# Performance work log

Measured on AMD Instinct MI355X. Metric: run time of the kernel, lower is better.

The kernel has to match this reference:

```python
import jax, jax.numpy as jnp
import numpy as np

IMG_LEN, TXT_LEN = 50, 76
SEQ = IMG_LEN + TXT_LEN
D_IMG, D, VOCAB = 768, 512, 49408
N_LAYERS = 2
EPS = 1e-5


def _layer_norm(x, g, b):
    m = jnp.mean(x, axis=-1, keepdims=True)
    v = jnp.mean(jnp.square(x - m), axis=-1, keepdims=True)
    return (x - m) * jax.lax.rsqrt(v + EPS) * g + b


def setup_inputs() -> dict:
    key = jax.random.key(0)
    ks = jax.random.split(key, 20)
    s = 0.02
    inp = {
        "image_embeddings": jax.random.normal(ks[0], (32, IMG_LEN, D_IMG), jnp.float32),
        "caption_ids": jax.random.randint(ks[1], (32, TXT_LEN), 0, VOCAB),
        "token_emb": jax.random.normal(ks[2], (VOCAB, D), jnp.float32) * s,
        "pos_emb": jax.random.normal(ks[3], (TXT_LEN, D), jnp.float32) * s,
        "ff0_w": jax.random.normal(ks[4], (D_IMG, D), jnp.float32) * s,
        "ff0_b": jnp.zeros((D,), jnp.float32),
        "wq": jax.random.normal(ks[5], (D, D), jnp.float32) * s,
        "wq_b": jnp.zeros((D,), jnp.float32),
        "wk": jax.random.normal(ks[6], (D, D), jnp.float32) * s,
        "wk_b": jnp.zeros((D,), jnp.float32),
        "wv": jax.random.normal(ks[7], (D, D), jnp.float32) * s,
        "wv_b": jnp.zeros((D,), jnp.float32),
        "ln_g": jnp.ones((D,), jnp.float32),
        "ln_b": jnp.zeros((D,), jnp.float32),
        "ff1_w": jax.random.normal(ks[8], (D, D), jnp.float32) * s,
        "ff1_b": jnp.zeros((D,), jnp.float32),
        "ff2_w": jax.random.normal(ks[9], (D, VOCAB), jnp.float32) * s,
        "ff2_b": jnp.zeros((VOCAB,), jnp.float32),
    }
    return inp


def reference(image_embeddings, caption_ids, token_emb, pos_emb, ff0_w, ff0_b,
              wq, wq_b, wk, wk_b, wv, wv_b, ln_g, ln_b, ff1_w, ff1_b, ff2_w, ff2_b):
    # prefix-causal mask: fully visible image prefix, causal over the rest
    mask = jnp.tril(jnp.ones((SEQ, SEQ), jnp.float32)).at[:, :IMG_LEN].set(1.0)

    img = image_embeddings @ ff0_w + ff0_b                      # [B,50,512]
    txt = token_emb[caption_ids] + pos_emb[None, :, :]          # [B,76,512]
    x = jnp.concatenate([img, txt], axis=1)                     # [B,126,512]
    x = _layer_norm(x, ln_g, ln_b)

    for _ in range(N_LAYERS):  # shared params across layers (as in source)
        res1 = x
        q = x @ wq + wq_b
        k = x @ wk + wk_b
        v = x @ wv + wv_b
        sims = jnp.einsum('bqd,bkd->bqk', q, k) / np.sqrt(D).astype(np.float32)
        sims = jnp.where(mask == 0, -1e9, sims)
        attn = jax.nn.softmax(sims, axis=-1)
        x = jnp.einsum('bqk,bkd->bqd', attn, v)
        x = _layer_norm(x + res1, ln_g, ln_b)
        res2 = x
        x = x @ ff1_w + ff1_b
        x = _layer_norm(x + res2, ln_g, ln_b)

    logits = x @ ff2_w + ff2_b                                  # [B,126,VOCAB]
    return logits[:, IMG_LEN:, :]                               # [B,76,VOCAB]
```

## Files before the change

### kernel.cpp

```cpp
#include <hip/hip_runtime.h>

typedef unsigned short ushort_t;
typedef __attribute__((ext_vector_type(8))) short short8;
typedef __attribute__((ext_vector_type(4))) float f32x4;
typedef __attribute__((ext_vector_type(4))) unsigned short bf4;
typedef __attribute__((ext_vector_type(8))) unsigned short bf8v;

__device__ __forceinline__ ushort_t f2bf(float f) {
    union { float f; unsigned u; } v; v.f = f;
    unsigned r = v.u + 0x7FFFu + ((v.u >> 16) & 1u);
    return (ushort_t)(r >> 16);
}

__device__ __forceinline__ void g2lds16(const ushort_t* g, ushort_t* l) {
    __builtin_amdgcn_global_load_lds(
        (const __attribute__((address_space(1))) void*)g,
        (__attribute__((address_space(3))) void*)l, 16, 0, 0);
}

#define LDT 72

__global__ __launch_bounds__(512) void gemm_big(
    const ushort_t* __restrict__ xb, const ushort_t* __restrict__ B,
    float* __restrict__ C, const float* __restrict__ bias,
    int K, int ldb, int ldc, int validM)
{
    __shared__ __attribute__((aligned(16))) ushort_t As[2][256 * 64];
    __shared__ __attribute__((aligned(16))) ushort_t Bs[2][256 * 64];

    const int tid = threadIdx.x;
    const int lane = tid & 63;
    const int wave = tid >> 6;
    const int wr = wave >> 2;
    const int wc = wave & 3;
    int tN, tM;
    {
        const int lin = blockIdx.x + blockIdx.y * gridDim.x;
        const int TM = gridDim.y;
        const int full = gridDim.x >> 3;
        const int per = TM << 3;
        const int g = lin / per;
        if (g < full) {
            const int rem = lin - g * per;
            tM = rem >> 3;
            tN = (g << 3) + (rem & 7);
        } else {
            const int rem = lin - full * per;
            const int w = gridDim.x - (full << 3);
            tM = rem / w;
            tN = (full << 3) + rem - tM * w;
        }
    }
    const int n0 = tN * 256;
    const ushort_t* Bbase = B + (long)n0 * ldb;

    f32x4 acc[8][4];
#pragma unroll
    for (int m = 0; m < 8; m++)
#pragma unroll
        for (int n = 0; n < 4; n++) acc[m][n] = (f32x4)0.f;

    auto STAGE = [&](int buf, int ks) {
#pragma unroll
        for (int i = 0; i < 4; i++) {
            int ch = i * 512 + tid;
            int row = ch >> 3, c16 = ch & 7;
            int c16s = c16 ^ (row & 7);
            int gr = tM * 256 + row;
            if (gr > 2431) gr = 2431;
            int bb = gr / 76;
            int xrow = bb * 126 + 50 + (gr - bb * 76);
            g2lds16(xb + (long)xrow * 512 + ks + (c16s << 3),
                    &As[buf][(i * 512 + wave * 64) * 8]);
        }
#pragma unroll
        for (int i = 0; i < 4; i++) {
            int ch = i * 512 + tid;
            int row = ch >> 3, c16 = ch & 7;
            int c16s = c16 ^ (row & 7);
            g2lds16(Bbase + (long)row * ldb + ks + (c16s << 3),
                    &Bs[buf][(i * 512 + wave * 64) * 8]);
        }
    };

    const int nt = K >> 6;
    STAGE(0, 0);
    for (int t = 0; t < nt; ++t) {
        if (t + 1 < nt) {
            STAGE((t + 1) & 1, (t + 1) << 6);
            asm volatile("s_waitcnt vmcnt(8)" ::: "memory");
        } else {
            asm volatile("s_waitcnt vmcnt(0)" ::: "memory");
        }
        asm volatile("s_barrier" ::: "memory");

        const ushort_t* Ac = As[t & 1];
        const ushort_t* Bc = Bs[t & 1];
        __builtin_amdgcn_s_setprio(1);
#pragma unroll
        for (int ksub = 0; ksub < 2; ksub++) {
            const int kk = ksub * 32 + ((lane >> 4) << 3);
            const int kc = kk >> 3;
            short8 af[8], bfr[4];
#pragma unroll
            for (int m = 0; m < 8; m++) {
                const int r = (wr << 7) + m * 16 + (lane & 15);
                af[m] = *(const short8*)(Ac + r * 64 + ((kc ^ (r & 7)) << 3));
            }
#pragma unroll
            for (int n = 0; n < 4; n++) {
                const int r = (wc << 6) + n * 16 + (lane & 15);
                bfr[n] = *(const short8*)(Bc + r * 64 + ((kc ^ (r & 7)) << 3));
            }
#pragma unroll
            for (int m = 0; m < 8; m++)
#pragma unroll
                for (int n = 0; n < 4; n++)
                    acc[m][n] = __builtin_amdgcn_mfma_f32_16x16x32_bf16(
                        af[m], bfr[n], acc[m][n], 0, 0, 0);
        }
        __builtin_amdgcn_s_setprio(0);
        asm volatile("s_barrier" ::: "memory");
    }

    const int rb = (wr << 7) + ((lane >> 4) << 2);
    const int cb = (wc << 6) + (lane & 15);
#pragma unroll
    for (int m = 0; m < 8; m++) {
#pragma unroll
        for (int i = 0; i < 4; i++) {
            int r = tM * 256 + rb + m * 16 + i;
            if (r >= validM) continue;
#pragma unroll
            for (int n = 0; n < 4; n++) {
                int cg = n0 + cb + n * 16;
                C[(long)r * ldc + cg] = acc[m][n][i] + bias[cg];
            }
        }
    }
}

__global__ __launch_bounds__(512) void ff1_fused(
    ushort_t* __restrict__ xbg, const ushort_t* __restrict__ ff1T,
    const float* __restrict__ bias, float* __restrict__ xg,
    const float* __restrict__ ln_g, const float* __restrict__ ln_b)
{
    __shared__ __attribute__((aligned(16))) ushort_t As[32 * 64];
    __shared__ __attribute__((aligned(16))) ushort_t Bs[512 * 64];
    __shared__ float redm[4 * 32];
    __shared__ float reds[4 * 32];

    const int tid = threadIdx.x;
    const int lane = tid & 63;
    const int wave = tid >> 6;
    const int wr = wave >> 2;
    const int wc = wave & 3;
    const int r0 = blockIdx.x << 5;

    f32x4 acc[8];
#pragma unroll
    for (int n = 0; n < 8; n++) acc[n] = (f32x4)0.f;

    auto STAGE = [&](int ks) {
#pragma unroll
        for (int i = 0; i < 9; i++) {
            int cb = i * 512 + wave * 64;
            if (cb >= 4352) continue;
            int ch = cb + lane;
            if (cb < 256) {
                int row = ch >> 3, c16 = ch & 7;
                int c16s = c16 ^ (row & 7);
                g2lds16(xbg + (long)(r0 + row) * 512 + ks + (c16s << 3),
                        &As[cb * 8]);
            } else {
                int bch = ch - 256;
                int row = bch >> 3, c16 = bch & 7;
                int c16s = c16 ^ (row & 7);
                g2lds16(ff1T + (long)row * 512 + ks + (c16s << 3),
                        &Bs[(cb - 256) * 8]);
            }
        }
    };

    for (int ks = 0; ks < 512; ks += 64) {
        if (ks) asm volatile("s_barrier" ::: "memory");
        STAGE(ks);
        asm volatile("s_waitcnt vmcnt(0)" ::: "memory");
        asm volatile("s_barrier" ::: "memory");

        __builtin_amdgcn_s_setprio(1);
#pragma unroll
        for (int ksub = 0; ksub < 2; ksub++) {
            const int kc = ksub * 4 + (lane >> 4);
            short8 af;
            {
                const int r = (wr << 4) + (lane & 15);
                af = *(const short8*)(As + r * 64 + ((kc ^ (r & 7)) << 3));
            }
            short8 bfr[8];
#pragma unroll
            for (int n = 0; n < 8; n++) {
                const int r = (wc << 7) + n * 16 + (lane & 15);
                bfr[n] = *(const short8*)(Bs + r * 64 + ((kc ^ (r & 7)) << 3));
            }
#pragma unroll
            for (int n = 0; n < 8; n++)
                acc[n] = __builtin_amdgcn_mfma_f32_16x16x32_bf16(
                    af, bfr[n], acc[n], 0, 0, 0);
        }
        __builtin_amdgcn_s_setprio(0);
    }

    float gg[8], bb2[8], bi[8];
#pragma unroll
    for (int n = 0; n < 8; n++) {
        int d = (wc << 7) + n * 16 + (lane & 15);
        gg[n] = ln_g[d];
        bb2[n] = ln_b[d];
        bi[n] = bias[d];
    }
    float vv[4][8];
#pragma unroll
    for (int i = 0; i < 4; i++) {
        const int rl = (wr << 4) + ((lane >> 4) << 2) + i;
        const long xrow = (long)(r0 + rl) << 9;
        float s = 0.f, sq = 0.f;
#pragma unroll
        for (int n = 0; n < 8; n++) {
            int d = (wc << 7) + n * 16 + (lane & 15);
            float v = acc[n][i] + bi[n] + xg[xrow + d];
            vv[i][n] = v;
            s += v; sq += v * v;
        }
#pragma unroll
        for (int o = 8; o >= 1; o >>= 1) { s += __shfl_xor(s, o); sq += __shfl_xor(sq, o); }
        if ((lane & 15) == 0) {
            redm[wc * 32 + rl] = s;
            reds[wc * 32 + rl] = sq;
        }
    }
    __syncthreads();
#pragma unroll
    for (int i = 0; i < 4; i++) {
        const int rl = (wr << 4) + ((lane >> 4) << 2) + i;
        float S = redm[rl] + redm[32 + rl] + redm[64 + rl] + redm[96 + rl];
        float SQ = reds[rl] + reds[32 + rl] + reds[64 + rl] + reds[96 + rl];
        float mean = S * (1.f / 512.f);
        float var = SQ * (1.f / 512.f) - mean * mean;
        float inv = rsqrtf(var + 1e-5f);
        const long xrow = (long)(r0 + rl) << 9;
#pragma unroll
        for (int n = 0; n < 8; n++) {
            int d = (wc << 7) + n * 16 + (lane & 15);
            float y = (vv[i][n] - mean) * inv * gg[n] + bb2[n];
            xg[xrow + d] = y;
            xbg[xrow + d] = f2bf(y);
        }
    }
}

__global__ __launch_bounds__(512) void attn_fused(
    const ushort_t* __restrict__ qkv, float* __restrict__ xg,
    ushort_t* __restrict__ xbg, const float* __restrict__ ln_g,
    const float* __restrict__ ln_b)
{
    __shared__ __attribute__((aligned(16))) ushort_t smem[41984];
    ushort_t* Vs = smem;
    ushort_t* Ps = smem + 32768;
    float* redm = (float*)(smem + 40960);
    float* reds = redm + 256;
    ushort_t* Qs = smem;
    ushort_t* Ks = smem + 8192;

    const int tid = threadIdx.x;
    const int lane = tid & 63;
    const int wave = tid >> 6;
    const int wr = wave >> 2;
    const int wc = wave & 3;
    const int qh = blockIdx.x;
    const int b  = blockIdx.y;
    const long qbase = ((long)(b * 126) + qh * 64) * 1536;
    const long kbase = (long)(b * 126) * 1536 + 512;
    const long vbase = (long)(b * 126) * 1536 + 1024;
    const float rsqd = 0.044194173824159216f;

    f32x4 acc[2][2];
#pragma unroll
    for (int m = 0; m < 2; m++)
#pragma unroll
        for (int n = 0; n < 2; n++) acc[m][n] = (f32x4)0.f;

    auto SQK = [&](int buf, int ks) {
        {
            int ch = tid;
            int row = ch >> 3, c16 = ch & 7;
            int c16s = c16 ^ (row & 7);
            g2lds16(qkv + qbase + (long)row * 1536 + ks + (c16s << 3),
                    Qs + buf * 4096 + (wave * 64) * 8);
        }
#pragma unroll
        for (int i = 0; i < 2; i++) {
            int ch = i * 512 + tid;
            int row = ch >> 3, c16 = ch & 7;
            int c16s = c16 ^ (row & 7);
            g2lds16(qkv + kbase + (long)row * 1536 + ks + (c16s << 3),
                    Ks + buf * 8192 + (i * 512 + wave * 64) * 8);
        }
    };

    SQK(0, 0);
    for (int t = 0; t < 8; ++t) {
        if (t < 7) {
            SQK((t + 1) & 1, (t + 1) << 6);
            asm volatile("s_waitcnt vmcnt(3)" ::: "memory");
        } else {
            asm volatile("s_waitcnt vmcnt(0)" ::: "memory");
        }
        asm volatile("s_barrier" ::: "memory");
        const ushort_t* Qc = Qs + (t & 1) * 4096;
        const ushort_t* Kc = Ks + (t & 1) * 8192;
#pragma unroll
        for (int ksub = 0; ksub < 2; ksub++) {
            const int kc = ksub * 4 + (lane >> 4);
            short8 af[2], bfr[2];
#pragma unroll
            for (int m = 0; m < 2; m++) {
                const int r = (wr << 5) + m * 16 + (lane & 15);
                af[m] = *(const short8*)(Qc + r * 64 + ((kc ^ (r & 7)) << 3));
            }
#pragma unroll
            for (int n = 0; n < 2; n++) {
                const int r = (wc << 5) + n * 16 + (lane & 15);
                bfr[n] = *(const short8*)(Kc + r * 64 + ((kc ^ (r & 7)) << 3));
            }
#pragma unroll
            for (int m = 0; m < 2; m++)
#pragma unroll
                for (int n = 0; n < 2; n++)
                    acc[m][n] = __builtin_amdgcn_mfma_f32_16x16x32_bf16(
                        af[m], bfr[n], acc[m][n], 0, 0, 0);
        }
        asm volatile("s_barrier" ::: "memory");
    }

    float rm[2][4];
#pragma unroll
    for (int m = 0; m < 2; m++) {
#pragma unroll
        for (int i = 0; i < 4; i++) {
            const int rl = (wr << 5) + m * 16 + ((lane >> 4) << 2) + i;
            const int q = qh * 64 + rl;
            float mx = -3.0e38f;
#pragma unroll
            for (int n = 0; n < 2; n++) {
                int j = (wc << 5) + n * 16 + (lane & 15);
                bool ok = (j < 126) && ((j < 50) || (j <= q));
                float s = acc[m][n][i] * rsqd;
                acc[m][n][i] = ok ? s : -3.0e38f;
                if (ok) mx = fmaxf(mx, s);
            }
#pragma unroll
            for (int o = 8; o >= 1; o >>= 1) mx = fmaxf(mx, __shfl_xor(mx, o));
            rm[m][i] = mx;
        }
    }
    if ((lane & 15) == 0) {
#pragma unroll
        for (int m = 0; m < 2; m++)
#pragma unroll
            for (int i = 0; i < 4; i++) {
                int rl = (wr << 5) + m * 16 + ((lane >> 4) << 2) + i;
                redm[wc * 64 + rl] = rm[m][i];
            }
    }
    __syncthreads();
    float rs[2][4];
#pragma unroll
    for (int m = 0; m < 2; m++) {
#pragma unroll
        for (int i = 0; i < 4; i++) {
            const int rl = (wr << 5) + m * 16 + ((lane >> 4) << 2) + i;
            float M = fmaxf(fmaxf(redm[rl], redm[64 + rl]),
                            fmaxf(redm[128 + rl], redm[192 + rl]));
            float sum = 0.f;
#pragma unroll
            for (int n = 0; n < 2; n++) {
                float s = acc[m][n][i];
                float e = (s > -1.0e37f) ? expf(s - M) : 0.f;
                acc[m][n][i] = e;
                sum += e;
            }
#pragma unroll
            for (int o = 8; o >= 1; o >>= 1) sum += __shfl_xor(sum, o);
            rs[m][i] = sum;
        }
    }
    if ((lane & 15) == 0) {
#pragma unroll
        for (int m = 0; m < 2; m++)
#pragma unroll
            for (int i = 0; i < 4; i++) {
                int rl = (wr << 5) + m * 16 + ((lane >> 4) << 2) + i;
                reds[wc * 64 + rl] = rs[m][i];
            }
    }
    __syncthreads();
#pragma unroll
    for (int m = 0; m < 2; m++) {
#pragma unroll
        for (int i = 0; i < 4; i++) {
            const int rl = (wr << 5) + m * 16 + ((lane >> 4) << 2) + i;
            float S = reds[rl] + reds[64 + rl] + reds[128 + rl] + reds[192 + rl];
            float inv = 1.f / S;
#pragma unroll
            for (int n = 0; n < 2; n++) {
                int j = (wc << 5) + n * 16 + (lane & 15);
                int c = j >> 3;
                Ps[rl * 128 + ((c ^ (rl & 7)) << 3) + (j & 7)] =
                    f2bf(acc[m][n][i] * inv);
            }
        }
    }
    __syncthreads();

    f32x4 po[2][8];
#pragma unroll
    for (int m = 0; m < 2; m++)
#pragma unroll
        for (int n = 0; n < 8; n++) po[m][n] = (f32x4)0.f;

    for (int jc = 0; jc < 2; jc++) {
#pragma unroll
        for (int q8 = 0; q8 < 16; q8++) {
            int qid = q8 * 512 + tid;
            int d = qid & 511, jq = qid >> 9;
            const ushort_t* vp = qkv + vbase + (long)(jc * 64 + jq * 4) * 1536 + d;
            bf4 p;
            p[0] = vp[0];
            p[1] = vp[1536];
            p[2] = vp[3072];
            p[3] = vp[4608];
            *(bf4*)(Vs + d * 64 + (((jq >> 1) ^ (d & 7)) << 3) + ((jq & 1) << 2)) = p;
        }
        __syncthreads();
#pragma unroll
        for (int ksub = 0; ksub < 2; ksub++) {
            const int kc = ksub * 4 + (lane >> 4);
            short8 af[2], bv[8];
#pragma unroll
            for (int m = 0; m < 2; m++) {
                const int r = (wr << 5) + m * 16 + (lane & 15);
                const int c = jc * 8 + kc;
                af[m] = *(const short8*)(Ps + r * 128 + ((c ^ (r & 7)) << 3));
            }
#pragma unroll
            for (int n = 0; n < 8; n++) {
                const int r = (wc << 7) + n * 16 + (lane & 15);
                bv[n] = *(const short8*)(Vs + r * 64 + ((kc ^ (r & 7)) << 3));
            }
#pragma unroll
            for (int m = 0; m < 2; m++)
#pragma unroll
                for (int n = 0; n < 8; n++)
                    po[m][n] = __builtin_amdgcn_mfma_f32_16x16x32_bf16(
                        af[m], bv[n], po[m][n], 0, 0, 0);
        }
        __syncthreads();
    }

    float gg[8], bb2[8];
#pragma unroll
    for (int n = 0; n < 8; n++) {
        int d = (wc << 7) + n * 16 + (lane & 15);
        gg[n] = ln_g[d];
        bb2[n] = ln_b[d];
    }
#pragma unroll
    for (int m = 0; m < 2; m++) {
#pragma unroll
        for (int i = 0; i < 4; i++) {
            const int rl = (wr << 5) + m * 16 + ((lane >> 4) << 2) + i;
            const int q = qh * 64 + rl;
            const long xrow = ((long)(b * 126 + q)) << 9;
            float s = 0.f, sq = 0.f;
#pragma unroll
            for (int n = 0; n < 8; n++) {
                int d = (wc << 7) + n * 16 + (lane & 15);
                float v = po[m][n][i] + xg[xrow + d];
                po[m][n][i] = v;
                s += v; sq += v * v;
            }
#pragma unroll
            for (int o = 8; o >= 1; o >>= 1) { s += __shfl_xor(s, o); sq += __shfl_xor(sq, o); }
            if ((lane & 15) == 0) {
                redm[wc * 64 + rl] = s;
                reds[wc * 64 + rl] = sq;
            }
        }
    }
    __syncthreads();
#pragma unroll
    for (int m = 0; m < 2; m++) {
#pragma unroll
        for (int i = 0; i < 4; i++) {
            const int rl = (wr << 5) + m * 16 + ((lane >> 4) << 2) + i;
            const int q = qh * 64 + rl;
            if (q >= 126) continue;
            float S = redm[rl] + redm[64 + rl] + redm[128 + rl] + redm[192 + rl];
            float SQ = reds[rl] + reds[64 + rl] + reds[128 + rl] + reds[192 + rl];
            float mean = S * (1.f / 512.f);
            float var = SQ * (1.f / 512.f) - mean * mean;
            float inv = rsqrtf(var + 1e-5f);
            const long xrow = ((long)(b * 126 + q)) << 9;
#pragma unroll
            for (int n = 0; n < 8; n++) {
                int d = (wc << 7) + n * 16 + (lane & 15);
                float y = (po[m][n][i] - mean) * inv * gg[n] + bb2[n];
                xg[xrow + d] = y;
                xbg[xrow + d] = f2bf(y);
            }
        }
    }
}

template <int BSRC, int SWZ, int NT>
__global__ __launch_bounds__(256) void gemm_bf16(
    const ushort_t* __restrict__ A, const void* __restrict__ Bv,
    float* __restrict__ C, ushort_t* __restrict__ Cb,
    const float* __restrict__ bias,
    int K, int lda, int ldb, int ldc,
    long sA, long sB, long sC,
    int validM, float scale)
{
    constexpr int LS = (BSRC == 0) ? 64 : LDT;
    constexpr int NBUF = (BSRC == 0) ? 2 : 1;
    __shared__ __attribute__((aligned(16))) ushort_t As[NBUF * 128 * LS];
    __shared__ __attribute__((aligned(16))) ushort_t Bs[NBUF * 128 * LS];

    const int tid = threadIdx.x;
    const int lane = tid & 63;
    const int wave = tid >> 6;
    const int wr = wave >> 1, wc = wave & 1;
    int tN = blockIdx.x, tM = blockIdx.y;
    const int bz = blockIdx.z;
    if (SWZ) {
        const int lin = blockIdx.x + blockIdx.y * gridDim.x;
        const int TM = gridDim.y;
        const int full = gridDim.x >> 3;
        const int per = TM << 3;
        const int g = lin / per;
        if (g < full) {
            const int rem = lin - g * per;
            tM = rem >> 3;
            tN = (g << 3) + (rem & 7);
        } else {
            const int rem = lin - full * per;
            const int w = gridDim.x - (full << 3);
            tM = rem / w;
            tN = (full << 3) + rem - tM * w;
        }
    }
    const int n0 = tN * 128;

    const ushort_t* Abase = A + (long)bz * sA + (long)tM * 128 * lda;
    const ushort_t* Bb = (BSRC == 0)
        ? (const ushort_t*)Bv + (long)bz * sB + (long)n0 * ldb : nullptr;
    const float* Bf = (BSRC == 1)
        ? (const float*)Bv + (long)bz * sB : nullptr;

    f32x4 acc[4][4];
#pragma unroll
    for (int m = 0; m < 4; m++)
#pragma unroll
        for (int n = 0; n < 4; n++) acc[m][n] = (f32x4)0.f;

    if (BSRC == 0) {
        auto STAGE = [&](int buf, int ks) {
            ushort_t* Ad = As + buf * (128 * 64);
            ushort_t* Bd = Bs + buf * (128 * 64);
#pragma unroll
            for (int i = 0; i < 4; i++) {
                int ch = wave * 256 + i * 64 + lane;
                int row = ch >> 3, c16 = ch & 7;
                int c16s = c16 ^ (row & 7);
                g2lds16(Abase + (long)row * lda + ks + (c16s << 3),
                        Ad + (wave * 256 + i * 64) * 8);
            }
#pragma unroll
            for (int i = 0; i < 4; i++) {
                int ch = wave * 256 + i * 64 + lane;
                int row = ch >> 3, c16 = ch & 7;
                int c16s = c16 ^ (row & 7);
                g2lds16(Bb + (long)row * ldb + ks + (c16s << 3),
                        Bd + (wave * 256 + i * 64) * 8);
            }
        };

        const int nt = K >> 6;
        STAGE(0, 0);
        for (int t = 0; t < nt; ++t) {
            if (t + 1 < nt) {
                STAGE((t + 1) & 1, (t + 1) << 6);
                asm volatile("s_waitcnt vmcnt(8)" ::: "memory");
            } else {
                asm volatile("s_waitcnt vmcnt(0)" ::: "memory");
            }
            asm volatile("s_barrier" ::: "memory");

            const ushort_t* Ac = As + (t & 1) * (128 * 64);
            const ushort_t* Bc = Bs + (t & 1) * (128 * 64);
#pragma unroll
            for (int ksub = 0; ksub < 2; ksub++) {
                const int kk = ksub * 32 + ((lane >> 4) << 3);
                const int kc = kk >> 3;
                short8 af[4], bfr[4];
#pragma unroll
                for (int m = 0; m < 4; m++) {
                    const int r = (wr << 6) + m * 16 + (lane & 15);
                    af[m] = *(const short8*)(Ac + r * 64 + ((kc ^ (r & 7)) << 3));
                }
#pragma unroll
                for (int n = 0; n < 4; n++) {
                    const int r = (wc << 6) + n * 16 + (lane & 15);
                    bfr[n] = *(const short8*)(Bc + r * 64 + ((kc ^ (r & 7)) << 3));
                }
#pragma unroll
                for (int m = 0; m < 4; m++)
#pragma unroll
                    for (int n = 0; n < 4; n++)
                        acc[m][n] = __builtin_amdgcn_mfma_f32_16x16x32_bf16(
                            af[m], bfr[n], acc[m][n], 0, 0, 0);
            }
            asm volatile("s_barrier" ::: "memory");
        }
    } else {
        for (int ks = 0; ks < K; ks += 64) {
            short8 ar[4];
#pragma unroll
            for (int i = 0; i < 4; i++) {
                int ch = wave * 256 + i * 64 + lane;
                int row = ch >> 3, c16 = ch & 7;
                ar[i] = *(const short8*)(Abase + (long)row * lda + ks + (c16 << 3));
            }
            bf4 pk[8];
#pragma unroll
            for (int q = 0; q < 8; q++) {
                int qid = q * 256 + tid;
                int n = qid & 127, kq = qid >> 7;
                const float* wp = Bf + (long)(ks + kq * 4) * ldb + n0 + n;
                bf4 p;
                p[0] = f2bf(wp[0]);
                p[1] = f2bf(wp[ldb]);
                p[2] = f2bf(wp[2 * (long)ldb]);
                p[3] = f2bf(wp[3 * (long)ldb]);
                pk[q] = p;
            }
            if (ks) __syncthreads();
#pragma unroll
            for (int i = 0; i < 4; i++) {
                int ch = wave * 256 + i * 64 + lane;
                int row = ch >> 3, c16 = ch & 7;
                *(short8*)(As + row * LS + (c16 << 3)) = ar[i];
            }
#pragma unroll
            for (int q = 0; q < 8; q++) {
                int qid = q * 256 + tid;
                int n = qid & 127, kq = qid >> 7;
                *(bf4*)(Bs + n * LS + (kq << 2)) = pk[q];
            }
            __syncthreads();

#pragma unroll
            for (int ksub = 0; ksub < 2; ksub++) {
                const int kk = ksub * 32 + ((lane >> 4) << 3);
                short8 af[4], bfr[4];
#pragma unroll
                for (int m = 0; m < 4; m++) {
                    const int r = (wr << 6) + m * 16 + (lane & 15);
                    af[m] = *(const short8*)(As + r * LS + kk);
                }
#pragma unroll
                for (int n = 0; n < 4; n++) {
                    const int r = (wc << 6) + n * 16 + (lane & 15);
                    bfr[n] = *(const short8*)(Bs + r * LS + kk);
                }
#pragma unroll
                for (int m = 0; m < 4; m++)
#pragma unroll
                    for (int n = 0; n < 4; n++)
                        acc[m][n] = __builtin_amdgcn_mfma_f32_16x16x32_bf16(
                            af[m], bfr[n], acc[m][n], 0, 0, 0);
            }
            if (ks + 64 < K) __syncthreads();
        }
    }

    const int rb = (wr << 6) + ((lane >> 4) << 2);
    const int cb = (wc << 6) + (lane & 15);
#pragma unroll
    for (int m = 0; m < 4; m++) {
#pragma unroll
        for (int i = 0; i < 4; i++) {
            int r = tM * 128 + rb + m * 16 + i;
            if (r >= validM) continue;
#pragma unroll
            for (int n = 0; n < 4; n++) {
                int cg = n0 + cb + n * 16;
                float v = acc[m][n][i] * scale + (bias ? bias[cg] : 0.f);
                long off = (long)bz * sC + (long)r * ldc + cg;
                if (C) {
                    if (NT) __builtin_nontemporal_store(v, &C[off]);
                    else    C[off] = v;
                }
                if (Cb) Cb[off] = f2bf(v);
            }
        }
    }
}

__global__ __launch_bounds__(256) void transpose_bf(
    const float* __restrict__ in, ushort_t* __restrict__ out, int R, int C)
{
    __shared__ float t[32][33];
    int c0 = blockIdx.x << 5, r0 = blockIdx.y << 5;
    int tx = threadIdx.x, ty = threadIdx.y;
#pragma unroll
    for (int i = 0; i < 4; i++)
        t[ty + i * 8][tx] = in[(long)(r0 + ty + i * 8) * C + c0 + tx];
    __syncthreads();
#pragma unroll
    for (int i = 0; i < 4; i++)
        out[(long)(c0 + ty + i * 8) * R + r0 + tx] = f2bf(t[tx][ty + i * 8]);
}

__global__ __launch_bounds__(256) void transpose_ff2(
    const float* __restrict__ in, ushort_t* __restrict__ out)
{
    __shared__ float t[64][65];
    const int c0 = blockIdx.x << 6;
    const int r0 = blockIdx.y << 6;
    const int tx = threadIdx.x & 63, ty = threadIdx.x >> 6;
#pragma unroll
    for (int i = 0; i < 16; i++) {
        int r = ty + i * 4;
        t[r][tx] = in[(long)(r0 + r) * 49408 + c0 + tx];
    }
    __syncthreads();
#pragma unroll
    for (int i = 0; i < 16; i++) {
        int r = ty + i * 4;
        out[(long)(c0 + r) * 512 + r0 + tx] = f2bf(t[tx][r]);
    }
}

__global__ __launch_bounds__(256) void transpose_bf3(
    const float* __restrict__ s0, const float* __restrict__ s1,
    const float* __restrict__ s2, ushort_t* __restrict__ out)
{
    __shared__ float t[32][33];
    const float* in = (blockIdx.z == 0) ? s0 : (blockIdx.z == 1) ? s1 : s2;
    ushort_t* o = out + (long)blockIdx.z * 512 * 512;
    int c0 = blockIdx.x << 5, r0 = blockIdx.y << 5;
    int tx = threadIdx.x, ty = threadIdx.y;
#pragma unroll
    for (int i = 0; i < 4; i++)
        t[ty + i * 8][tx] = in[(long)(r0 + ty + i * 8) * 512 + c0 + tx];
    __syncthreads();
#pragma unroll
    for (int i = 0; i < 4; i++)
        o[(long)(c0 + ty + i * 8) * 512 + r0 + tx] = f2bf(t[tx][ty + i * 8]);
}

__global__ __launch_bounds__(256) void biascat(
    const float* __restrict__ b0, const float* __restrict__ b1,
    const float* __restrict__ b2, float* __restrict__ out)
{
    int i = blockIdx.x * 256 + threadIdx.x;
    const float* s = (i < 512) ? b0 : (i < 1024) ? b1 : b2;
    out[i] = s[i & 511];
}

__global__ __launch_bounds__(256) void conv_pad(
    const float* __restrict__ in, ushort_t* __restrict__ out,
    int validR, int C, int total)
{
    int idx = blockIdx.x * 256 + threadIdx.x;
    if (idx >= total) return;
    int r = idx / C;
    float v = 0.f;
    if (r < validR) v = in[idx];
    out[idx] = f2bf(v);
}

__global__ __launch_bounds__(256) void gather_txt(
    const ushort_t* __restrict__ xb, ushort_t* __restrict__ At)
{
    int idx = blockIdx.x * 256 + threadIdx.x;
    if (idx >= 2560 * 512) return;
    int r = idx >> 9, c = idx & 511;
    if (r < 2432) {
        int b = r / 76, t = r - b * 76;
        At[idx] = xb[((long)(b * 126 + 50 + t) << 9) + c];
    } else {
        At[idx] = 0;
    }
}

__global__ __launch_bounds__(64) void build_x(
    const float* __restrict__ imgout, const int* __restrict__ cap,
    const float* __restrict__ tok, const float* __restrict__ pos,
    const float* __restrict__ g, const float* __restrict__ bb,
    float* __restrict__ x, ushort_t* __restrict__ xb)
{
    int r = blockIdx.x, lane = threadIdx.x;
    int c0 = lane << 3;
    long base = ((long)r << 9) + c0;
    if (r >= 4032) {
        *(f32x4*)(x + base) = (f32x4)0.f;
        *(f32x4*)(x + base + 4) = (f32x4)0.f;
        *(bf8v*)(xb + base) = (bf8v)0;
        return;
    }
    int b = r / 126, s = r - b * 126;
    float v[8];
    if (s < 50) {
        const float* src = imgout + ((long)(b * 50 + s) << 9) + c0;
        f32x4 a0 = *(const f32x4*)src, a1 = *(const f32x4*)(src + 4);
#pragma unroll
        for (int i = 0; i < 4; i++) { v[i] = a0[i]; v[4 + i] = a1[i]; }
    } else {
        int t = s - 50;
        int id = cap[b * 76 + t];
        const float* s1 = tok + ((long)id << 9) + c0;
        const float* s2 = pos + ((long)t << 9) + c0;
        f32x4 a0 = *(const f32x4*)s1, a1 = *(const f32x4*)(s1 + 4);
        f32x4 b0 = *(const f32x4*)s2, b1 = *(const f32x4*)(s2 + 4);
#pragma unroll
        for (int i = 0; i < 4; i++) { v[i] = a0[i] + b0[i]; v[4 + i] = a1[i] + b1[i]; }
    }
    float sum = 0.f, sq = 0.f;
#pragma unroll
    for (int i = 0; i < 8; i++) { sum += v[i]; sq += v[i] * v[i]; }
#pragma unroll
    for (int o = 32; o >= 1; o >>= 1) { sum += __shfl_xor(sum, o); sq += __shfl_xor(sq, o); }
    float mean = sum * (1.f / 512.f);
    float var = sq * (1.f / 512.f) - mean * mean;
    float inv = rsqrtf(var + 1e-5f);
    bf8v ob;
#pragma unroll
    for (int i = 0; i < 8; i++) {
        float y = (v[i] - mean) * inv * g[c0 + i] + bb[c0 + i];
        x[base + i] = y;
        ob[i] = f2bf(y);
    }
    *(bf8v*)(xb + base) = ob;
}

extern "C" void kernel_launch(void* const* d_in, const int* in_sizes, int n_in,
                              void* d_out, int out_size, void* d_ws, size_t ws_size,
                              hipStream_t stream)
{
    const float* img   = (const float*)d_in[0];
    const int*   cap   = (const int*)  d_in[1];
    const float* tok   = (const float*)d_in[2];
    const float* pos   = (const float*)d_in[3];
    const float* ff0_w = (const float*)d_in[4];
    const float* ff0_b = (const float*)d_in[5];
    const float* wq    = (const float*)d_in[6];
    const float* wq_b  = (const float*)d_in[7];
    const float* wk    = (const float*)d_in[8];
    const float* wk_b  = (const float*)d_in[9];
    const float* wv    = (const float*)d_in[10];
    const float* wv_b  = (const float*)d_in[11];
    const float* ln_g  = (const float*)d_in[12];
    const float* ln_b  = (const float*)d_in[13];
    const float* ff1_w = (const float*)d_in[14];
    const float* ff1_b = (const float*)d_in[15];
    const float* ff2_w = (const float*)d_in[16];
    const float* ff2_b = (const float*)d_in[17];

    char* ws = (char*)d_ws;
    size_t o = 0;
    auto alloc = [&](size_t bytes) { size_t r = o; o += (bytes + 255) & ~(size_t)255; return r; };

    float*    x     = (float*)   (ws + alloc(4096ull * 512 * 4));
    ushort_t* xb    = (ushort_t*)(ws + alloc(4096ull * 512 * 2));
    float*    tmpf  = (float*)   (ws + alloc(4096ull * 512 * 4));
    ushort_t* qkvb  = (ushort_t*)(ws + alloc(4096ull * 1536 * 2));
    ushort_t* Atxt  = (ushort_t*)(ws + alloc(2560ull * 512 * 2));
    ushort_t* Aimg  = (ushort_t*)(ws + alloc(1664ull * 768 * 2));
    ushort_t* wqkvT = (ushort_t*)(ws + alloc(1536ull * 512 * 2));
    ushort_t* ff0T  = (ushort_t*)(ws + alloc(512ull * 768 * 2));
    ushort_t* ff1T  = (ushort_t*)(ws + alloc(512ull * 512 * 2));
    float*    bcat  = (float*)   (ws + alloc(1536 * 4));
    size_t base_bytes = o;
    size_t ff2T_bytes = 49408ull * 512 * 2;
    bool use_ff2T = (ws_size >= base_bytes + ff2T_bytes + 256);
    ushort_t* ff2T = use_ff2T ? (ushort_t*)(ws + alloc(ff2T_bytes)) : nullptr;

    dim3 b32x8(32, 8);

    transpose_bf3<<<dim3(16, 16, 3), b32x8, 0, stream>>>(wq, wk, wv, wqkvT);
    transpose_bf<<<dim3(16, 24), b32x8, 0, stream>>>(ff0_w, ff0T, 768, 512);
    transpose_bf<<<dim3(16, 16), b32x8, 0, stream>>>(ff1_w, ff1T, 512, 512);
    biascat<<<6, 256, 0, stream>>>(wq_b, wk_b, wv_b, bcat);
    if (use_ff2T)
        transpose_ff2<<<dim3(772, 8), 256, 0, stream>>>(ff2_w, ff2T);
    conv_pad<<<(1664 * 768 + 255) / 256, 256, 0, stream>>>(img, Aimg, 1600, 768, 1664 * 768);

    gemm_bf16<0, 0, 0><<<dim3(4, 13, 1), 256, 0, stream>>>(
        Aimg, ff0T, tmpf, nullptr, ff0_b, 768, 768, 768, 512, 0, 0, 0, 1600, 1.f);

    build_x<<<4096, 64, 0, stream>>>(tmpf, cap, tok, pos, ln_g, ln_b, x, xb);

    for (int l = 0; l < 2; l++) {
        gemm_bf16<0, 0, 0><<<dim3(12, 32, 1), 256, 0, stream>>>(
            xb, wqkvT, nullptr, qkvb, bcat, 512, 512, 512, 1536, 0, 0, 0, 4096, 1.f);
        attn_fused<<<dim3(2, 32), 512, 0, stream>>>(qkvb, x, xb, ln_g, ln_b);
        ff1_fused<<<126, 512, 0, stream>>>(xb, ff1T, ff1_b, x, ln_g, ln_b);
    }

    if (use_ff2T) {
        gemm_big<<<dim3(193, 10), 512, 0, stream>>>(
            xb, ff2T, (float*)d_out, ff2_b, 512, 512, 49408, 2432);
    } else {
        gather_txt<<<(2560 * 512 + 255) / 256, 256, 0, stream>>>(xb, Atxt);
        gemm_bf16<1, 1, 0><<<dim3(386, 20, 1), 256, 0, stream>>>(
            Atxt, ff2_w, (float*)d_out, nullptr, ff2_b, 512, 512, 49408, 49408,
            0, 0, 0, 2432, 1.f);
    }
}
```

Measured before the change: 437.1 us.

## Interleave next-tile global-to-LDS loads with MFMA phases in big GEMM

The next K-tile prefetch is split into four parts, each issued just before one quarter of the MFMA work on the current tile, instead of issuing the whole prefetch at the top of the iteration. The compute loop is restructured into four phases, each covering half of the M fragments and half of K, with setprio raised around each MFMA block. The aim is to spread memory instructions across the compute so the load queue and the MFMA pipe overlap better. In exchange, the wait at the top of each iteration now drains all outstanding loads (vmcnt(0)), which may expose latency if the prefetch is not finished in time. The B-fragment LDS reads are also repeated in each M-half.

After: 452.4 us. 1.03x slower.

```diff
diff --git a/kernel.cpp b/kernel.cpp
--- a/kernel.cpp
+++ b/kernel.cpp
@@ -83,43 +83,62 @@
         }
     };
 
+    auto STAGE_PART = [&](int buf, int ks, int p) {
+#pragma unroll
+        for (int ii = 0; ii < 2; ii++) {
+            int i = (p & 1) * 2 + ii;
+            int ch = i * 512 + tid;
+            int row = ch >> 3, c16 = ch & 7;
+            int c16s = c16 ^ (row & 7);
+            if (p < 2) {
+                int gr = tM * 256 + row;
+                if (gr > 2431) gr = 2431;
+                int bb = gr / 76;
+                int xrow = bb * 126 + 50 + (gr - bb * 76);
+                g2lds16(xb + (long)xrow * 512 + ks + (c16s << 3),
+                        &As[buf][(i * 512 + wave * 64) * 8]);
+            } else {
+                g2lds16(Bbase + (long)row * ldb + ks + (c16s << 3),
+                        &Bs[buf][(i * 512 + wave * 64) * 8]);
+            }
+        }
+    };
+
     const int nt = K >> 6;
     STAGE(0, 0);
     for (int t = 0; t < nt; ++t) {
-        if (t + 1 < nt) {
-            STAGE((t + 1) & 1, (t + 1) << 6);
-            asm volatile("s_waitcnt vmcnt(8)" ::: "memory");
-        } else {
-            asm volatile("s_waitcnt vmcnt(0)" ::: "memory");
-        }
+        asm volatile("s_waitcnt vmcnt(0)" ::: "memory");
         asm volatile("s_barrier" ::: "memory");
 
         const ushort_t* Ac = As[t & 1];
         const ushort_t* Bc = Bs[t & 1];
-        __builtin_amdgcn_s_setprio(1);
-#pragma unroll
-        for (int ksub = 0; ksub < 2; ksub++) {
-            const int kk = ksub * 32 + ((lane >> 4) << 3);
+#pragma unroll
+        for (int p = 0; p < 4; p++) {
+            if (t + 1 < nt) STAGE_PART((t + 1) & 1, (t + 1) << 6, p);
+            const int mh = p >> 1;
+            const int ks2 = p & 1;
+            const int kk = ks2 * 32 + ((lane >> 4) << 3);
             const int kc = kk >> 3;
-            short8 af[8], bfr[4];
-#pragma unroll
-            for (int m = 0; m < 8; m++) {
-                const int r = (wr << 7) + m * 16 + (lane & 15);
-                af[m] = *(const short8*)(Ac + r * 64 + ((kc ^ (r & 7)) << 3));
+            short8 af[4], bfr[4];
+#pragma unroll
+            for (int mi = 0; mi < 4; mi++) {
+                const int r = (wr << 7) + (mh * 4 + mi) * 16 + (lane & 15);
+                af[mi] = *(const short8*)(Ac + r * 64 + ((kc ^ (r & 7)) << 3));
             }
 #pragma unroll
             for (int n = 0; n < 4; n++) {
                 const int r = (wc << 6) + n * 16 + (lane & 15);
                 bfr[n] = *(const short8*)(Bc + r * 64 + ((kc ^ (r & 7)) << 3));
             }
-#pragma unroll
-            for (int m = 0; m < 8; m++)
+            __builtin_amdgcn_s_setprio(1);
+#pragma unroll
+            for (int mi = 0; mi < 4; mi++)
 #pragma unroll
                 for (int n = 0; n < 4; n++)
-                    acc[m][n] = __builtin_amdgcn_mfma_f32_16x16x32_bf16(
-                        af[m], bfr[n], acc[m][n], 0, 0, 0);
-        }
-        __builtin_amdgcn_s_setprio(0);
+                    acc[mh * 4 + mi][n] = __builtin_amdgcn_mfma_f32_16x16x32_bf16(
+                        af[mi], bfr[n], acc[mh * 4 + mi][n], 0, 0, 0);
+            __builtin_amdgcn_s_setprio(0);
+        }
         asm volatile("s_barrier" ::: "memory");
     }
 
```
